# Optimization experiments

Measured on AMD Instinct MI355X. Metric: run time of the kernel, lower is better.

The kernel has to match this reference:

```python
import jax, jax.numpy as jnp
import numpy as np
from jax import lax


def setup_inputs() -> dict:
    key = jax.random.key(0)
    ks = jax.random.split(key, 9)
    B = 4096
    x = jax.random.normal(ks[0], (B, 1, 28, 28), jnp.float32)

    def init(k, shape, fan_in):
        return (jax.random.normal(k, shape, jnp.float32) / np.float32(np.sqrt(fan_in)))

    W1 = init(ks[1], (32, 1, 3, 3), 1 * 9)
    b1 = init(ks[2], (32,), 1 * 9)
    W2 = init(ks[3], (64, 32, 3, 3), 32 * 9)
    b2 = init(ks[4], (64,), 32 * 9)
    Wl1 = init(ks[5], (14 * 14 * 64, 128), 14 * 14 * 64)
    bl1 = init(ks[6], (128,), 14 * 14 * 64)
    Wl2 = init(ks[7], (128, 10), 128)
    bl2 = init(ks[8], (10,), 128)
    return {"x": x, "W1": W1, "b1": b1, "W2": W2, "b2": b2,
            "Wl1": Wl1, "bl1": bl1, "Wl2": Wl2, "bl2": bl2}


def _conv_same(h, W, b):
    # submanifold sparse conv == SAME-padded dense conv, output restricted to active sites
    y = lax.conv_general_dilated(h, W, window_strides=(1, 1), padding="SAME",
                                 dimension_numbers=("NCHW", "OIHW", "NCHW"))
    return y + b[None, :, None, None]


def reference(x, W1, b1, W2, b2, Wl1, bl1, Wl2, bl2):
    # active-site mask from Voxels.from_dense (nonzero pixels); submanifold convs keep it fixed
    mask = (jnp.abs(x) > 0).any(axis=1, keepdims=True).astype(x.dtype)  # [B,1,28,28]
    h = jax.nn.relu(_conv_same(x, W1, b1) * mask)   # [B,32,28,28]
    h = jax.nn.relu(_conv_same(h, W2, b2) * mask)   # [B,64,28,28]
    # sparse 2x2/2 max pool; inactive sites are 0 and post-ReLU actives are >=0,
    # so dense window max == sparse max, and all-inactive windows densify to 0
    B = h.shape[0]
    h = h.reshape(B, 64, 14, 2, 14, 2).max(axis=(3, 5))  # [B,64,14,14]
    h = h.reshape(B, 64 * 14 * 14)
    # dropout is identity in eval
    h = jax.nn.relu(h @ Wl1 + bl1)
    logits = h @ Wl2 + bl2
    return jax.nn.log_softmax(logits, axis=1)
```

## Files before the change

kernel.cpp:

```cpp
#include <hip/hip_runtime.h>
#include <math.h>

typedef __bf16 bf16;
typedef __bf16 bf16x4 __attribute__((ext_vector_type(4)));
typedef __bf16 bf16x8 __attribute__((ext_vector_type(8)));
typedef unsigned short u16;
typedef unsigned short u16x4 __attribute__((ext_vector_type(4)));
typedef unsigned short u16x8 __attribute__((ext_vector_type(8)));
typedef float f32x4 __attribute__((ext_vector_type(4)));
typedef float f32x16 __attribute__((ext_vector_type(16)));
typedef unsigned int u32x4 __attribute__((ext_vector_type(4)));

__global__ void prep_all(const float* __restrict__ W2, bf16* __restrict__ w2r,
                         const float* __restrict__ W1, bf16* __restrict__ w1f,
                         const float* __restrict__ Wl1, bf16* __restrict__ wl1t) {
    __shared__ float tile[32 * 129];
    const int b = blockIdx.x;
    const int t = threadIdx.x;
    if (b < 392) {
        const int s  = b >> 1;
        const int cg = b & 1;
        for (int e = t; e < 4096; e += 256) {
            int cl = e >> 7, n = e & 127;
            tile[cl * 129 + n] = Wl1[((long)(cg * 32 + cl) * 196 + s) * 128 + n];
        }
        __syncthreads();
        for (int e = t; e < 4096; e += 256) {
            int n = e >> 5, cl = e & 31;
            wl1t[(long)n * 12544 + s * 64 + cg * 32 + cl] = (bf16)tile[cl * 129 + n];
        }
    } else {
        int e = (b - 392) * 256 + t;
        if (e < 18432) {
            int j  = e & 7;
            int l  = (e >> 3) & 63;
            int f  = e >> 9;
            int s  = f >> 1;
            int nt = f & 1;
            int tap  = s >> 1;
            int ci   = (s & 1) * 16 + (l >> 5) * 8 + j;
            int cout = nt * 32 + (l & 31);
            w2r[e] = (bf16)W2[cout * 288 + ci * 9 + tap];
        } else {
            int e2 = e - 18432;
            if (e2 < 512) {
                int j = e2 & 7;
                int l = e2 >> 3;
                int k = (l >> 5) * 8 + j;
                int n = l & 31;
                w1f[e2] = (k < 9) ? (bf16)W1[n * 9 + k] : (bf16)0.f;
            }
        }
    }
}

__global__ __launch_bounds__(256, 3)
void conv_fused(const float* __restrict__ x, const float* __restrict__ b1,
                const bf16* __restrict__ w2r, const bf16* __restrict__ w1f,
                const float* __restrict__ b2, bf16* __restrict__ pooled)
{
    __shared__ __attribute__((aligned(16))) bf16  h1s[16 * 1032];
    __shared__ __attribute__((aligned(16))) float mneg[98 * 4];
    __shared__ __attribute__((aligned(16))) bf16  xs[640];

    const int t    = threadIdx.x;
    const int lane = t & 63;
    const int wv   = t >> 6;
    const int img  = blockIdx.x >> 1;
    const int hb   = blockIdx.x & 1;
    const int nt   = wv & 1;
    const int wp   = wv >> 1;
    const int ml31 = lane & 31;
    const int lg   = lane >> 5;

    const float* xi = x + img * 784;

    bf16x8 breg[18];
    {
        const bf16x8* wp2 = (const bf16x8*)w2r;
        #pragma unroll
        for (int s = 0; s < 18; s++)
            breg[s] = wp2[(2 * s + nt) * 64 + lane];
    }
    const bf16x8 w1frag = *(const bf16x8*)&w1f[lane * 8];
    const float  bias2  = b2[nt * 32 + ml31];
    f32x4 bq[4];
    #pragma unroll
    for (int run = 0; run < 4; run++)
        bq[run] = *(const f32x4*)&b1[4 * lg + 8 * run];

    for (int e = t; e < 640; e += 256) {
        int j  = e >> 5;
        int c  = e & 31;
        int xr = hb * 14 - 2 + j;
        int xc = c - 1;
        float v = 0.f;
        if (xr >= 0 && xr < 28 && xc >= 0 && xc < 28) v = xi[xr * 28 + xc];
        xs[e] = (bf16)v;
    }
    __syncthreads();

    const u16* xu = (const u16*)xs;

    for (int e = t; e < 392; e += 256) {
        int s   = e >> 2, q = e & 3;
        int spi = s / 14, spj = s - spi * 14;
        u16 cv = xu[(2 * spi + (q >> 1) + 2) * 32 + 2 * spj + (q & 1) + 1];
        mneg[e] = ((cv & 0x7fff) != 0) ? 0.f : -1e30f;
    }

    #pragma unroll 1
    for (int Mt = wv; Mt < 16; Mt += 4) {
        const int bb = Mt * 32 + ml31 - 1;
        u16x8 tv;
        if (lg == 0) {
            tv[0] = xu[bb];      tv[1] = xu[bb + 1];  tv[2] = xu[bb + 2];
            tv[3] = xu[bb + 32]; tv[4] = xu[bb + 33]; tv[5] = xu[bb + 34];
            tv[6] = xu[bb + 64]; tv[7] = xu[bb + 65];
        } else {
            #pragma unroll
            for (int j = 0; j < 8; j++) tv[j] = 0;
            tv[0] = xu[bb + 66];
        }
        bf16x8 af = *(bf16x8*)&tv;

        f32x16 acc;
        #pragma unroll
        for (int run = 0; run < 4; run++)
            #pragma unroll
            for (int j = 0; j < 4; j++) acc[run * 4 + j] = bq[run][j];
        acc = __builtin_amdgcn_mfma_f32_32x32x16_bf16(w1frag, af, acc, 0, 0, 0);

        u16 ctr = xu[(Mt + 1) * 32 + ml31];
        const bool ok = (ml31 >= 1) && (ml31 <= 28) && ((ctr & 0x7fff) != 0);
        const int wbase = Mt * 1032 + ml31 * 32;
        const int swz   = (ml31 & 6) << 2;
        #pragma unroll
        for (int run = 0; run < 4; run++) {
            bf16x4 w4;
            #pragma unroll
            for (int j = 0; j < 4; j++) {
                float s = acc[run * 4 + j];
                w4[j] = (bf16)(ok ? fmaxf(s, 0.f) : 0.f);
            }
            const int ci0 = 4 * lg + 8 * run;
            *(bf16x4*)&h1s[wbase + (ci0 ^ swz)] = w4;
        }
    }
    __syncthreads();

    const int cib = lg * 8;

    int q  = ml31 & 3;
    int pj = wp * 8 + (ml31 >> 2);
    int pi = 0;
    if (pj >= 14) { pj -= 14; pi = 1; }

    bf16* pout = pooled + (long)img * 12544 + hb * 98 * 64 + nt * 32 + ml31;

    #pragma unroll 1
    for (int Mt = wp; Mt < 13; Mt += 2) {
        int row = 2 * pi + (q >> 1);
        if (row > 13) row = 13;
        int colb = 2 * pj + (q & 1);
        int rowb = row * 1032;

        int e0a[3], e1a[3];
        #pragma unroll
        for (int dc = 0; dc < 3; dc++) {
            int cc   = colb + dc;
            int swz  = (cc & 6) << 2;
            int base = rowb + cc * 32;
            e0a[dc] = base + (cib ^ swz);
            e1a[dc] = base + ((16 + cib) ^ swz);
        }

        f32x16 acc;
        #pragma unroll
        for (int e = 0; e < 16; e++) acc[e] = bias2;

        #pragma unroll
        for (int dr = 0; dr < 3; dr++) {
            #pragma unroll
            for (int dc = 0; dc < 3; dc++) {
                const int tap = dr * 3 + dc;
                bf16x8 a0 = *(const bf16x8*)&h1s[e0a[dc] + dr * 1032];
                bf16x8 a1 = *(const bf16x8*)&h1s[e1a[dc] + dr * 1032];
                acc = __builtin_amdgcn_mfma_f32_32x32x16_bf16(a0, breg[2 * tap],     acc, 0, 0, 0);
                acc = __builtin_amdgcn_mfma_f32_32x32x16_bf16(a1, breg[2 * tap + 1], acc, 0, 0, 0);
            }
        }

        int slg = 8 * Mt + lg;
        #pragma unroll
        for (int gg = 0; gg < 4; gg++) {
            if (slg < 98) {
                f32x4 mn = *(const f32x4*)&mneg[slg * 4];
                float v0 = acc[gg * 4 + 0] + mn[0];
                float v1 = acc[gg * 4 + 1] + mn[1];
                float v2 = acc[gg * 4 + 2] + mn[2];
                float v3 = acc[gg * 4 + 3] + mn[3];
                float pm = fmaxf(fmaxf(v0, v1), fmaxf(v2, v3));
                pout[slg * 64] = (bf16)fmaxf(pm, 0.f);
            }
            slg += 2;
        }

        pj += 2; if (pj >= 14) { pj -= 14; pi += 1; }
        pi += 1;
    }
}

__global__ __launch_bounds__(256, 4)
void fc1(const bf16* __restrict__ pooled, const bf16* __restrict__ wl1t,
         float* __restrict__ part)
{
    __shared__ __attribute__((aligned(16))) bf16 As[2][32 * 64];
    __shared__ __attribute__((aligned(16))) bf16 Bs[2][128 * 64];

    const int t    = threadIdx.x;
    const int lane = t & 63;
    const int wv   = t >> 6;
    const int ml   = lane & 15;
    const int kg   = lane >> 4;
    const int wm   = wv & 1;
    const int wn   = wv >> 1;
    const int m0   = blockIdx.x * 32;
    const int ks   = blockIdx.y;
    const int k0   = ks * 1792;

    const bf16* asrc;
    {
        int sub = t >> 7, i = t & 127;
        int r  = i >> 2;
        int jq = (i & 3) ^ ((r >> 1) & 3);
        asrc = pooled + (long)(m0 + r) * 12544 + k0 + sub * 32 + jq * 8;
    }
    const bf16* bsrc[4];
    #pragma unroll
    for (int u = 0; u < 4; u++) {
        int c  = u * 256 + t;
        int sub = c >> 9, i = c & 511;
        int r  = i >> 2;
        int jq = (i & 3) ^ ((r >> 1) & 3);
        bsrc[u] = wl1t + (long)r * 12544 + k0 + sub * 32 + jq * 8;
    }

    const int am = wm * 16 + ml;
    int aoff[2], boff[4];
    #pragma unroll
    for (int s = 0; s < 2; s++)
        aoff[s] = s * 1024 + ((am * 32 + kg * 8) ^ ((am & 6) << 2));
    #pragma unroll
    for (int j = 0; j < 4; j++) {
        int n = wn * 64 + j * 16 + ml;
        boff[j] = (n * 32 + kg * 8) ^ ((n & 6) << 2);
    }

    f32x4 acc[4];
    {
        f32x4 z = {0.f, 0.f, 0.f, 0.f};
        #pragma unroll
        for (int j = 0; j < 4; j++) acc[j] = z;
    }

    u32x4 ra = *(const u32x4*)asrc;
    u32x4 rb[4];
    #pragma unroll
    for (int u = 0; u < 4; u++) rb[u] = *(const u32x4*)bsrc[u];
    *(u32x4*)&As[0][t * 8] = ra;
    #pragma unroll
    for (int u = 0; u < 4; u++) *(u32x4*)&Bs[0][(u * 256 + t) * 8] = rb[u];

    for (int kt = 0; kt < 28; kt++) {
        __syncthreads();
        const int cur = kt & 1;
        if (kt < 27) {
            const int kb = (kt + 1) * 64;
            ra = *(const u32x4*)(asrc + kb);
            #pragma unroll
            for (int u = 0; u < 4; u++) rb[u] = *(const u32x4*)(bsrc[u] + kb);
        }
        #pragma unroll
        for (int s = 0; s < 2; s++) {
            bf16x8 af = *(const bf16x8*)&As[cur][aoff[s]];
            #pragma unroll
            for (int j = 0; j < 4; j++) {
                bf16x8 bf = *(const bf16x8*)&Bs[cur][s * 4096 + boff[j]];
                acc[j] = __builtin_amdgcn_mfma_f32_16x16x32_bf16(af, bf, acc[j], 0, 0, 0);
            }
        }
        if (kt < 27) {
            *(u32x4*)&As[cur ^ 1][t * 8] = ra;
            #pragma unroll
            for (int u = 0; u < 4; u++)
                *(u32x4*)&Bs[cur ^ 1][(u * 256 + t) * 8] = rb[u];
        }
    }

    float* pp = part + ((long)ks * 4096 + m0 + wm * 16) * 128 + wn * 64;
    #pragma unroll
    for (int j = 0; j < 4; j++)
        #pragma unroll
        for (int r = 0; r < 4; r++)
            pp[(kg * 4 + r) * 128 + j * 16 + ml] = acc[j][r];
}

__global__ __launch_bounds__(256)
void fc2_lsm(const float* __restrict__ part, const float* __restrict__ bl1,
             const float* __restrict__ Wl2, const float* __restrict__ bl2,
             float* __restrict__ out)
{
    const int wv   = threadIdx.x >> 6;
    const int lane = threadIdx.x & 63;
    const int img  = blockIdx.x * 4 + wv;
    const float* pb = part + (long)img * 128;

    float ac[10];
    #pragma unroll
    for (int c = 0; c < 10; c++) ac[c] = 0.f;

    #pragma unroll
    for (int u = 0; u < 2; u++) {
        int n = lane + 64 * u;
        float s = bl1[n];
        #pragma unroll
        for (int k = 0; k < 7; k++) s += pb[(long)k * 4096 * 128 + n];
        float h = s > 0.f ? s : 0.f;
        #pragma unroll
        for (int c = 0; c < 10; c++) ac[c] += h * Wl2[n * 10 + c];
    }
    #pragma unroll
    for (int o = 32; o > 0; o >>= 1)
        #pragma unroll
        for (int c = 0; c < 10; c++) ac[c] += __shfl_down(ac[c], o, 64);

    if (lane == 0) {
        float lg[10], mx = -1e30f;
        #pragma unroll
        for (int c = 0; c < 10; c++) {
            lg[c] = ac[c] + bl2[c];
            mx = lg[c] > mx ? lg[c] : mx;
        }
        float se = 0.f;
        #pragma unroll
        for (int c = 0; c < 10; c++) se += __expf(lg[c] - mx);
        float ls = __logf(se);
        #pragma unroll
        for (int c = 0; c < 10; c++) out[img * 10 + c] = lg[c] - mx - ls;
    }
}

extern "C" void kernel_launch(void* const* d_in, const int* in_sizes, int n_in,
                              void* d_out, int out_size, void* d_ws, size_t ws_size,
                              hipStream_t stream) {
    const float* x   = (const float*)d_in[0];
    const float* W1  = (const float*)d_in[1];
    const float* b1  = (const float*)d_in[2];
    const float* W2  = (const float*)d_in[3];
    const float* b2  = (const float*)d_in[4];
    const float* Wl1 = (const float*)d_in[5];
    const float* bl1 = (const float*)d_in[6];
    const float* Wl2 = (const float*)d_in[7];
    const float* bl2 = (const float*)d_in[8];
    float* out = (float*)d_out;

    char* ws = (char*)d_ws;
    bf16*  w2r    = (bf16*)ws;
    bf16*  w1f    = (bf16*)(ws + 40960);
    bf16*  wl1t   = (bf16*)(ws + 65536);
    bf16*  pooled = (bf16*)(ws + 65536 + 4194304);
    float* part   = (float*)(ws + 65536 + 4194304 + 102760448);

    prep_all  <<<466,            256, 0, stream>>>(W2, w2r, W1, w1f, Wl1, wl1t);
    conv_fused<<<8192,           256, 0, stream>>>(x, b1, w2r, w1f, b2, pooled);
    fc1       <<<dim3(128, 7),   256, 0, stream>>>(pooled, wl1t, part);
    fc2_lsm   <<<1024,           256, 0, stream>>>(part, bl1, Wl2, bl2, out);
}
```

Before: 252.6 us.

## Compute both conv2 output-channel tiles per wave to reuse A fragments

Each wave now covers all 64 output channels, holding both N-tiles of conv2 weights in registers (36 fragments) and running two accumulators, instead of splitting channel halves across waves. Each A fragment loaded from LDS feeds two MFMAs, halving LDS reads per MFMA, and the M-tiles are spread across all 4 waves. Register pressure roughly doubles for weights and accumulators, so the occupancy hint is lowered from 3 to 2 blocks per CU, which weakens latency hiding.

```diff
diff --git a/kernel.cpp b/kernel.cpp
--- a/kernel.cpp
+++ b/kernel.cpp
@@ -54,7 +54,7 @@
     }
 }
 
-__global__ __launch_bounds__(256, 3)
+__global__ __launch_bounds__(256, 2)
 void conv_fused(const float* __restrict__ x, const float* __restrict__ b1,
                 const bf16* __restrict__ w2r, const bf16* __restrict__ w1f,
                 const float* __restrict__ b2, bf16* __restrict__ pooled)
@@ -68,22 +68,21 @@
     const int wv   = t >> 6;
     const int img  = blockIdx.x >> 1;
     const int hb   = blockIdx.x & 1;
-    const int nt   = wv & 1;
-    const int wp   = wv >> 1;
     const int ml31 = lane & 31;
     const int lg   = lane >> 5;
 
     const float* xi = x + img * 784;
 
-    bf16x8 breg[18];
+    bf16x8 breg[36];
     {
         const bf16x8* wp2 = (const bf16x8*)w2r;
         #pragma unroll
-        for (int s = 0; s < 18; s++)
-            breg[s] = wp2[(2 * s + nt) * 64 + lane];
+        for (int f = 0; f < 36; f++)
+            breg[f] = wp2[f * 64 + lane];
     }
     const bf16x8 w1frag = *(const bf16x8*)&w1f[lane * 8];
-    const float  bias2  = b2[nt * 32 + ml31];
+    const float  bias2A = b2[ml31];
+    const float  bias2B = b2[32 + ml31];
     f32x4 bq[4];
     #pragma unroll
     for (int run = 0; run < 4; run++)
@@ -152,14 +151,15 @@
     const int cib = lg * 8;
 
     int q  = ml31 & 3;
-    int pj = wp * 8 + (ml31 >> 2);
+    int pj = wv * 8 + (ml31 >> 2);
     int pi = 0;
-    if (pj >= 14) { pj -= 14; pi = 1; }
-
-    bf16* pout = pooled + (long)img * 12544 + hb * 98 * 64 + nt * 32 + ml31;
+    if (pj >= 14) { pj -= 14; pi += 1; }
+    if (pj >= 14) { pj -= 14; pi += 1; }
+
+    bf16* pout = pooled + (long)img * 12544 + hb * 98 * 64 + ml31;
 
     #pragma unroll 1
-    for (int Mt = wp; Mt < 13; Mt += 2) {
+    for (int Mt = wv; Mt < 13; Mt += 4) {
         int row = 2 * pi + (q >> 1);
         if (row > 13) row = 13;
         int colb = 2 * pj + (q & 1);
@@ -175,9 +175,9 @@
             e1a[dc] = base + ((16 + cib) ^ swz);
         }
 
-        f32x16 acc;
-        #pragma unroll
-        for (int e = 0; e < 16; e++) acc[e] = bias2;
+        f32x16 accA, accB;
+        #pragma unroll
+        for (int e = 0; e < 16; e++) { accA[e] = bias2A; accB[e] = bias2B; }
 
         #pragma unroll
         for (int dr = 0; dr < 3; dr++) {
@@ -186,8 +186,10 @@
                 const int tap = dr * 3 + dc;
                 bf16x8 a0 = *(const bf16x8*)&h1s[e0a[dc] + dr * 1032];
                 bf16x8 a1 = *(const bf16x8*)&h1s[e1a[dc] + dr * 1032];
-                acc = __builtin_amdgcn_mfma_f32_32x32x16_bf16(a0, breg[2 * tap],     acc, 0, 0, 0);
-                acc = __builtin_amdgcn_mfma_f32_32x32x16_bf16(a1, breg[2 * tap + 1], acc, 0, 0, 0);
+                accA = __builtin_amdgcn_mfma_f32_32x32x16_bf16(a0, breg[4 * tap + 0], accA, 0, 0, 0);
+                accB = __builtin_amdgcn_mfma_f32_32x32x16_bf16(a0, breg[4 * tap + 1], accB, 0, 0, 0);
+                accA = __builtin_amdgcn_mfma_f32_32x32x16_bf16(a1, breg[4 * tap + 2], accA, 0, 0, 0);
+                accB = __builtin_amdgcn_mfma_f32_32x32x16_bf16(a1, breg[4 * tap + 3], accB, 0, 0, 0);
             }
         }
 
@@ -196,18 +198,24 @@
         for (int gg = 0; gg < 4; gg++) {
             if (slg < 98) {
                 f32x4 mn = *(const f32x4*)&mneg[slg * 4];
-                float v0 = acc[gg * 4 + 0] + mn[0];
-                float v1 = acc[gg * 4 + 1] + mn[1];
-                float v2 = acc[gg * 4 + 2] + mn[2];
-                float v3 = acc[gg * 4 + 3] + mn[3];
-                float pm = fmaxf(fmaxf(v0, v1), fmaxf(v2, v3));
-                pout[slg * 64] = (bf16)fmaxf(pm, 0.f);
+                float a0 = accA[gg * 4 + 0] + mn[0];
+                float a1 = accA[gg * 4 + 1] + mn[1];
+                float a2 = accA[gg * 4 + 2] + mn[2];
+                float a3 = accA[gg * 4 + 3] + mn[3];
+                float pmA = fmaxf(fmaxf(a0, a1), fmaxf(a2, a3));
+                pout[slg * 64] = (bf16)fmaxf(pmA, 0.f);
+                float c0 = accB[gg * 4 + 0] + mn[0];
+                float c1 = accB[gg * 4 + 1] + mn[1];
+                float c2 = accB[gg * 4 + 2] + mn[2];
+                float c3 = accB[gg * 4 + 3] + mn[3];
+                float pmB = fmaxf(fmaxf(c0, c1), fmaxf(c2, c3));
+                pout[slg * 64 + 32] = (bf16)fmaxf(pmB, 0.f);
             }
             slg += 2;
         }
 
-        pj += 2; if (pj >= 14) { pj -= 14; pi += 1; }
-        pi += 1;
+        pj += 4; if (pj >= 14) { pj -= 14; pi += 1; }
+        pi += 2;
     }
 }
 
```

Result: slower. 276.8 us (+9.6%).
